# Kernel tuning notes

Measured on AMD Instinct MI355X. Metric: run time of the kernel, lower is better.

The kernel has to match this reference:

```python
import jax, jax.numpy as jnp
import numpy as np

N_HEAD = 16

def setup_inputs() -> dict:
    key = jax.random.key(0)
    k1, k2, k3, k4, k5 = jax.random.split(key, 5)
    B, T, C = 8, 2048, 1024
    hs = C // N_HEAD  # 64
    return {
        "ids": jax.random.normal(k1, (B, T, C), dtype=jnp.float32),
        "qkv_w": jax.random.normal(k2, (3 * hs, C), dtype=jnp.float32) * (C ** -0.5),
        "qkv_b": jax.random.normal(k3, (3 * hs,), dtype=jnp.float32) * 0.02,
        "proj_w": jax.random.normal(k4, (C, C), dtype=jnp.float32) * (C ** -0.5),
        "proj_b": jax.random.normal(k5, (C,), dtype=jnp.float32) * 0.02,
    }

def reference(ids, qkv_w, qkv_b, proj_w, proj_b):
    B, T, C = ids.shape
    hs = qkv_w.shape[0] // 3  # head_size
    # All heads share the same qkv Linear (input is replicated per-head in the
    # original), so compute one head and tile at the end.
    qkv = ids @ qkv_w.T + qkv_b                      # [B,T,3*hs]
    q, k, v = jnp.split(qkv, 3, axis=-1)             # each [B,T,hs]
    wei = jnp.einsum('btd,bsd->bts', q, k)           # [B,T,T]
    tril = jnp.tril(jnp.ones((T, T), dtype=bool))
    wei = jnp.where(tril, wei, jnp.float32(0.0))     # causal mask (no softmax)
    out_h = jnp.einsum('bts,bsd->btd', wei, v)       # [B,T,hs]
    out = jnp.tile(out_h, (1, 1, N_HEAD))            # identical heads concatenated
    return out @ proj_w.T + proj_b                   # [B,T,C]
```

## Files before the change

kernel.cpp:

```cpp
#include <hip/hip_runtime.h>
#include <hip/hip_bf16.h>

#define Bsz 8
#define Tsz 2048
#define Csz 1024
#define HSsz 64
#define NQ 192

typedef __attribute__((ext_vector_type(8))) short short8v;
typedef __attribute__((ext_vector_type(4))) float f32x4;
typedef unsigned short ushortT;
typedef unsigned int uintT;

__device__ __forceinline__ unsigned int f2bf(float f) {
    union { float f; unsigned int u; } v; v.f = f;
    return (v.u + 0x7fffu + ((v.u >> 16) & 1u)) >> 16;
}

__device__ __forceinline__ unsigned int pk2bf(float lo, float hi) {
    union { __hip_bfloat162 h2; unsigned int u; } cv;
    cv.h2 = __float22bfloat162_rn(float2{lo, hi});
    return cv.u;
}

__global__ __launch_bounds__(256) void k_prep(const float* __restrict__ qw,
                                              const float* __restrict__ pw,
                                              ushortT* __restrict__ wB,
                                              ushortT* __restrict__ w2a) {
    const int blk = blockIdx.x;
    if (blk < 96) {
        int idx = blk * 256 + threadIdx.x;
        int l = idx & 63;
        int ksjt = idx >> 6;
        int jt = ksjt % 12, ks = ksjt / 12;
        int j = jt * 16 + (l & 15);
        int k = ks * 32 + (l >> 4) * 8;
        const float* src = &qw[j * Csz + k];
        float4 a = *(const float4*)src;
        float4 b = *(const float4*)(src + 4);
        uint4 o;
        o.x = f2bf(a.x) | (f2bf(a.y) << 16);
        o.y = f2bf(a.z) | (f2bf(a.w) << 16);
        o.z = f2bf(b.x) | (f2bf(b.y) << 16);
        o.w = f2bf(b.z) | (f2bf(b.w) << 16);
        *(uint4*)&wB[(size_t)idx * 8] = o;
    } else {
        int idx = (blk - 96) * 256 + threadIdx.x;
        int l = idx & 63;
        int rest = idx >> 6;
        int m = rest & 63, ks = rest >> 6;
        int c = m * 16 + (l & 15);
        int d0 = ks * 32 + (l >> 4) * 8;
        float s0 = 0, s1 = 0, s2 = 0, s3 = 0, s4 = 0, s5 = 0, s6 = 0, s7 = 0;
#pragma unroll
        for (int hh = 0; hh < 16; ++hh) {
            const float* p = &pw[c * Csz + hh * HSsz + d0];
            float4 x = *(const float4*)p;
            float4 y = *(const float4*)(p + 4);
            s0 += x.x; s1 += x.y; s2 += x.z; s3 += x.w;
            s4 += y.x; s5 += y.y; s6 += y.z; s7 += y.w;
        }
        uint4 o;
        o.x = f2bf(s0) | (f2bf(s1) << 16);
        o.y = f2bf(s2) | (f2bf(s3) << 16);
        o.z = f2bf(s4) | (f2bf(s5) << 16);
        o.w = f2bf(s6) | (f2bf(s7) << 16);
        *(uint4*)&w2a[(size_t)idx * 8] = o;
    }
}

__global__ __launch_bounds__(512, 4) void k_qkv_mfma(const float* __restrict__ ids,
                                                     const ushortT* __restrict__ wB,
                                                     const float* __restrict__ bias,
                                                     ushortT* __restrict__ Qf,
                                                     ushortT* __restrict__ Kf,
                                                     ushortT* __restrict__ Vf) {
    __shared__ float sA[2][32 * 132];
    uintT* Lqk = (uintT*)&sA[0][0];
    uintT* Lv  = Lqk + 32 * 68;

    const int tid = threadIdx.x;
    const int wv  = tid >> 6;
    const int l   = tid & 63;
    const int wm  = wv >> 2;
    const int wn  = wv & 3;
    const int lg  = l >> 4, ll = l & 15;

    const int row0 = blockIdx.x * 32;

    const int srow = tid >> 4;
    const int scol = (tid & 15) * 8;
    const float* gsrc = ids + (size_t)(row0 + srow) * Csz + scol;

    const int afrow = wm * 16 + ll;

    f32x4 acc[3];
    acc[0] = acc[1] = acc[2] = (f32x4){0.f, 0.f, 0.f, 0.f};

    float4 st0 = *(const float4*)gsrc;
    float4 st1 = *(const float4*)(gsrc + 4);

    const ushortT* bbase_p = wB + ((size_t)(wn * 3) * 64 + l) * 8;

    for (int c = 0; c < 8; ++c) {
        float* bufp = &sA[c & 1][0];
        float* wp = &bufp[srow * 132 + scol];
        *(float4*)wp = st0;
        *(float4*)(wp + 4) = st1;
        __syncthreads();
        if (c < 7) {
            st0 = *(const float4*)(gsrc + (c + 1) * 128);
            st1 = *(const float4*)(gsrc + (c + 1) * 128 + 4);
        }
#pragma unroll
        for (int kk = 0; kk < 4; ++kk) {
            const ushortT* bp = bbase_p + (size_t)(4 * c + kk) * 6144;
            short8v b0 = *(const short8v*)(bp);
            short8v b1 = *(const short8v*)(bp + 512);
            short8v b2 = *(const short8v*)(bp + 1024);

            const float* ap = &bufp[afrow * 132 + kk * 32 + lg * 8];
            float4 a0 = *(const float4*)ap;
            float4 a1 = *(const float4*)(ap + 4);
            union { short8v s; unsigned int u[4]; } af;
            af.u[0] = pk2bf(a0.x, a0.y); af.u[1] = pk2bf(a0.z, a0.w);
            af.u[2] = pk2bf(a1.x, a1.y); af.u[3] = pk2bf(a1.z, a1.w);

            acc[0] = __builtin_amdgcn_mfma_f32_16x16x32_bf16(af.s, b0, acc[0], 0, 0, 0);
            acc[1] = __builtin_amdgcn_mfma_f32_16x16x32_bf16(af.s, b1, acc[1], 0, 0, 0);
            acc[2] = __builtin_amdgcn_mfma_f32_16x16x32_bf16(af.s, b2, acc[2], 0, 0, 0);
        }
    }
    __syncthreads();

    const int crow_l = wm * 16 + lg * 4;
    ushortT* L16 = (ushortT*)Lqk;
#pragma unroll
    for (int n = 0; n < 3; ++n) {
        const int jb = wn * 3 + n;
        const int j  = jb * 16 + ll;
        const float bj = bias[j];
        float v0 = acc[n][0] + bj, v1 = acc[n][1] + bj;
        float v2 = acc[n][2] + bj, v3 = acc[n][3] + bj;
        if (jb < 8) {
            ushortT* p = &L16[crow_l * 136 + j];
            p[0]   = (ushortT)f2bf(v0);
            p[136] = (ushortT)f2bf(v1);
            p[272] = (ushortT)f2bf(v2);
            p[408] = (ushortT)f2bf(v3);
        } else {
            uintT* p = &Lv[(j - 128) * 20 + (crow_l >> 1)];
            p[0] = pk2bf(v0, v1);
            p[1] = pk2bf(v2, v3);
        }
    }
    __syncthreads();

    const int l2 = tid & 63, ll2 = l2 & 15, lg2 = l2 >> 4;
    if (tid < 256) {
        const int ks = (tid >> 6) & 1, m = tid >> 7;
        uint4 q = *(const uint4*)&Lqk[(m * 16 + ll2) * 68 + ks * 16 + lg2 * 4];
        *(uint4*)&Qf[(((size_t)(row0 >> 4) + m) * 2 + ks) * 512 + l2 * 8] = q;
        const int n = tid >> 6;
        uint4 v = *(const uint4*)&Lv[(n * 16 + ll2) * 20 + lg2 * 4];
        const int bb = row0 >> 11, s32 = (row0 >> 5) & 63;
        *(uint4*)&Vf[((((size_t)bb * 64 + s32) * 4 + n) * 64 + l2) * 8] = v;
    } else {
        const int ks = (tid >> 6) & 1, m = (tid >> 7) & 1;
        uint4 k = *(const uint4*)&Lqk[(m * 16 + ll2) * 68 + 32 + ks * 16 + lg2 * 4];
        *(uint4*)&Kf[(((size_t)(row0 >> 4) + m) * 2 + ks) * 512 + l2 * 8] = k;
    }
}

__global__ __launch_bounds__(256, 3) void k_attn_mfma(const ushortT* __restrict__ Qf,
                                                      const ushortT* __restrict__ Kf,
                                                      const ushortT* __restrict__ Vf,
                                                      ushortT* __restrict__ hf) {
    __shared__ uintT su[4 * 2 * 16 * 36];
    __shared__ float s_o[4][32 * 68];

    const int tid = threadIdx.x;
    const int w  = tid >> 6;
    const int l  = tid & 63;
    const int lg = l >> 4;
    const int ll = l & 15;

    const int u = blockIdx.x;
    const int b = u & 7;
    const int si = 63 - (u >> 3);

    const int nT  = (si >> 1) + 1;
    const int qn  = nT >> 2, rem = nT & 3;
    const int t0  = w * qn + (w < rem ? w : rem);
    const int cnt = qn + (w < rem ? 1 : 0);

    const int gq = b * 128 + si * 2;

    short8v qf[2][2];
#pragma unroll
    for (int mt = 0; mt < 2; ++mt)
#pragma unroll
        for (int ks = 0; ks < 2; ++ks)
            qf[mt][ks] = *(const short8v*)&Qf[(((size_t)gq + mt) * 2 + ks) * 512 + l * 8];

    f32x4 oacc[2][4];
#pragma unroll
    for (int mt = 0; mt < 2; ++mt)
#pragma unroll
        for (int n = 0; n < 4; ++n) oacc[mt][n] = (f32x4){0.f, 0.f, 0.f, 0.f};

    for (int tile = t0; tile < t0 + cnt; ++tile) {
        const int gs = b * 128 + tile * 4;
        short8v kf[4][2];
#pragma unroll
        for (int ms = 0; ms < 4; ++ms) {
            const ushortT* kp = &Kf[(((size_t)gs + ms) * 2) * 512 + l * 8];
            kf[ms][0] = *(const short8v*)kp;
            kf[ms][1] = *(const short8v*)(kp + 512);
        }
        f32x4 sacc[4][2];
#pragma unroll
        for (int ms = 0; ms < 4; ++ms)
#pragma unroll
            for (int mt = 0; mt < 2; ++mt) sacc[ms][mt] = (f32x4){0.f, 0.f, 0.f, 0.f};
#pragma unroll
        for (int ms = 0; ms < 4; ++ms)
#pragma unroll
            for (int mt = 0; mt < 2; ++mt) {
                sacc[ms][mt] = __builtin_amdgcn_mfma_f32_16x16x32_bf16(kf[ms][0], qf[mt][0], sacc[ms][mt], 0, 0, 0);
                sacc[ms][mt] = __builtin_amdgcn_mfma_f32_16x16x32_bf16(kf[ms][1], qf[mt][1], sacc[ms][mt], 0, 0, 0);
            }
        if (tile == nT - 1) {
#pragma unroll
            for (int ms = 0; ms < 4; ++ms)
#pragma unroll
                for (int mt = 0; mt < 2; ++mt) {
                    const int tg = si * 32 + mt * 16 + ll;
#pragma unroll
                    for (int rr2 = 0; rr2 < 4; ++rr2) {
                        int sg = tile * 64 + ms * 16 + 4 * lg + rr2;
                        if (sg > tg) sacc[ms][mt][rr2] = 0.f;
                    }
                }
        }
#pragma unroll
        for (int mt = 0; mt < 2; ++mt)
#pragma unroll
            for (int ms = 0; ms < 4; ++ms) {
                uint2 pk;
                pk.x = pk2bf(sacc[ms][mt][0], sacc[ms][mt][1]);
                pk.y = pk2bf(sacc[ms][mt][2], sacc[ms][mt][3]);
                *(uint2*)&su[((w * 2 + mt) * 16 + ll) * 36 + ms * 8 + 2 * lg] = pk;
            }
        union { uint4 u4; short8v s; } pa[2][2];
#pragma unroll
        for (int mt = 0; mt < 2; ++mt)
#pragma unroll
            for (int h = 0; h < 2; ++h)
                pa[mt][h].u4 = *(const uint4*)&su[((w * 2 + mt) * 16 + ll) * 36 + h * 16 + lg * 4];

        const int gv = b * 64 + tile * 2;
        short8v vf[2][4];
#pragma unroll
        for (int h = 0; h < 2; ++h)
#pragma unroll
            for (int n = 0; n < 4; ++n)
                vf[h][n] = *(const short8v*)&Vf[((((size_t)gv + h) * 4 + n) * 64 + l) * 8];
#pragma unroll
        for (int mt = 0; mt < 2; ++mt)
#pragma unroll
            for (int n = 0; n < 4; ++n) {
                oacc[mt][n] = __builtin_amdgcn_mfma_f32_16x16x32_bf16(pa[mt][0].s, vf[0][n], oacc[mt][n], 0, 0, 0);
                oacc[mt][n] = __builtin_amdgcn_mfma_f32_16x16x32_bf16(pa[mt][1].s, vf[1][n], oacc[mt][n], 0, 0, 0);
            }
    }

#pragma unroll
    for (int mt = 0; mt < 2; ++mt)
#pragma unroll
        for (int n = 0; n < 4; ++n)
#pragma unroll
            for (int rr2 = 0; rr2 < 4; ++rr2)
                s_o[w][(mt * 16 + 4 * lg + rr2) * 68 + 16 * n + ll] = oacc[mt][n][rr2];
    __syncthreads();

    const int l2 = tid & 63, ll2 = l2 & 15, lg2 = l2 >> 4;
    const int ks = (tid >> 6) & 1, mt = tid >> 7;
    const int t = mt * 16 + ll2, dd = ks * 32 + lg2 * 8;
    float4 A = {0, 0, 0, 0}, B2 = {0, 0, 0, 0};
#pragma unroll
    for (int w2 = 0; w2 < 4; ++w2) {
        const float4 x = *(const float4*)&s_o[w2][t * 68 + dd];
        const float4 y = *(const float4*)&s_o[w2][t * 68 + dd + 4];
        A.x += x.x; A.y += x.y; A.z += x.z; A.w += x.w;
        B2.x += y.x; B2.y += y.y; B2.z += y.z; B2.w += y.w;
    }
    uint4 o;
    o.x = pk2bf(A.x, A.y);  o.y = pk2bf(A.z, A.w);
    o.z = pk2bf(B2.x, B2.y); o.w = pk2bf(B2.z, B2.w);
    *(uint4*)&hf[(((size_t)(b * 128 + si * 2) + mt) * 2 + ks) * 512 + l2 * 8] = o;
}

__global__ __launch_bounds__(256) void k_proj_mfma(const ushortT* __restrict__ hf,
                                                   const ushortT* __restrict__ w2a,
                                                   const float* __restrict__ pb,
                                                   float* __restrict__ out) {
    const int tid = threadIdx.x;
    const int w = tid >> 6, l = tid & 63;
    const size_t M0 = (size_t)blockIdx.x * 2;

    short8v hA0 = *(const short8v*)&hf[(M0 * 2 + 0) * 512 + l * 8];
    short8v hA1 = *(const short8v*)&hf[(M0 * 2 + 1) * 512 + l * 8];
    short8v hB0 = *(const short8v*)&hf[((M0 + 1) * 2 + 0) * 512 + l * 8];
    short8v hB1 = *(const short8v*)&hf[((M0 + 1) * 2 + 1) * 512 + l * 8];

    const int row = (l >> 4) * 4;
    const int tcol = l & 15;
    const size_t outA = (M0 * 16 + tcol) * Csz;
    const size_t outB = ((M0 + 1) * 16 + tcol) * Csz;

#pragma unroll 2
    for (int m = w * 16; m < w * 16 + 16; ++m) {
        const ushortT* ap = w2a + (size_t)(m * 64 + l) * 8;
        short8v a0 = *(const short8v*)ap;
        short8v a1 = *(const short8v*)(ap + 32768);
        const int c0 = m * 16 + row;
        const float4 pv = *(const float4*)&pb[c0];

        f32x4 accA = (f32x4){0.f, 0.f, 0.f, 0.f};
        accA = __builtin_amdgcn_mfma_f32_16x16x32_bf16(a0, hA0, accA, 0, 0, 0);
        accA = __builtin_amdgcn_mfma_f32_16x16x32_bf16(a1, hA1, accA, 0, 0, 0);
        f32x4 accB = (f32x4){0.f, 0.f, 0.f, 0.f};
        accB = __builtin_amdgcn_mfma_f32_16x16x32_bf16(a0, hB0, accB, 0, 0, 0);
        accB = __builtin_amdgcn_mfma_f32_16x16x32_bf16(a1, hB1, accB, 0, 0, 0);

        float4 oA, oB;
        oA.x = accA[0] + pv.x; oA.y = accA[1] + pv.y;
        oA.z = accA[2] + pv.z; oA.w = accA[3] + pv.w;
        oB.x = accB[0] + pv.x; oB.y = accB[1] + pv.y;
        oB.z = accB[2] + pv.z; oB.w = accB[3] + pv.w;
        *(float4*)&out[outA + c0] = oA;
        *(float4*)&out[outB + c0] = oB;
    }
}

extern "C" void kernel_launch(void* const* d_in, const int* in_sizes, int n_in,
                              void* d_out, int out_size, void* d_ws, size_t ws_size,
                              hipStream_t stream) {
    const float* ids    = (const float*)d_in[0];
    const float* qkv_w  = (const float*)d_in[1];
    const float* qkv_b  = (const float*)d_in[2];
    const float* proj_w = (const float*)d_in[3];
    const float* proj_b = (const float*)d_in[4];
    float* out = (float*)d_out;

    ushortT* Qf  = (ushortT*)d_ws;
    ushortT* Kf  = Qf + 16384 * HSsz;
    ushortT* Vf  = Kf + 16384 * HSsz;
    ushortT* hf  = Vf + 16384 * HSsz;
    ushortT* wB  = hf + 16384 * HSsz;
    ushortT* w2a = wB + 196608;

    hipLaunchKernelGGL(k_prep,      dim3(128), dim3(256), 0, stream, qkv_w, proj_w, wB, w2a);
    hipLaunchKernelGGL(k_qkv_mfma,  dim3(512), dim3(512), 0, stream, ids, wB, qkv_b, Qf, Kf, Vf);
    hipLaunchKernelGGL(k_attn_mfma, dim3(512), dim3(256), 0, stream, Qf, Kf, Vf, hf);
    hipLaunchKernelGGL(k_proj_mfma, dim3(512), dim3(256), 0, stream, hf, w2a, proj_b, out);
}
```

Measured before the change: 60.16 us.

## Double QKV row tile to 64 and stage activations as bf16 in LDS

```diff
diff --git a/kernel.cpp b/kernel.cpp
--- a/kernel.cpp
+++ b/kernel.cpp
@@ -75,60 +75,61 @@
                                                      ushortT* __restrict__ Qf,
                                                      ushortT* __restrict__ Kf,
                                                      ushortT* __restrict__ Vf) {
-    __shared__ float sA[2][32 * 132];
-    uintT* Lqk = (uintT*)&sA[0][0];
-    uintT* Lv  = Lqk + 32 * 68;
+    __shared__ uintT sA[2][64 * 68];
+    uintT* Lqk = &sA[0][0];
+    uintT* Lv  = Lqk + 64 * 68;
 
     const int tid = threadIdx.x;
     const int wv  = tid >> 6;
     const int l   = tid & 63;
-    const int wm  = wv >> 2;
-    const int wn  = wv & 3;
+    const int wm  = wv >> 1;
+    const int wn  = wv & 1;
     const int lg  = l >> 4, ll = l & 15;
 
-    const int row0 = blockIdx.x * 32;
-
-    const int srow = tid >> 4;
-    const int scol = (tid & 15) * 8;
+    const int row0 = blockIdx.x * 64;
+
+    const int srow = tid >> 3;
+    const int scol = (tid & 7) * 4;
     const float* gsrc = ids + (size_t)(row0 + srow) * Csz + scol;
+    const int swbase = srow * 68 + (scol >> 1);
 
     const int afrow = wm * 16 + ll;
 
-    f32x4 acc[3];
-    acc[0] = acc[1] = acc[2] = (f32x4){0.f, 0.f, 0.f, 0.f};
-
-    float4 st0 = *(const float4*)gsrc;
-    float4 st1 = *(const float4*)(gsrc + 4);
-
-    const ushortT* bbase_p = wB + ((size_t)(wn * 3) * 64 + l) * 8;
+    f32x4 acc[6];
+#pragma unroll
+    for (int n = 0; n < 6; ++n) acc[n] = (f32x4){0.f, 0.f, 0.f, 0.f};
+
+    float4 st[4];
+#pragma unroll
+    for (int j = 0; j < 4; ++j) st[j] = *(const float4*)(gsrc + j * 32);
+
+    const ushortT* bbase_p = wB + ((size_t)(wn * 6) * 64 + l) * 8;
 
     for (int c = 0; c < 8; ++c) {
-        float* bufp = &sA[c & 1][0];
-        float* wp = &bufp[srow * 132 + scol];
-        *(float4*)wp = st0;
-        *(float4*)(wp + 4) = st1;
+        uintT* bufp = &sA[c & 1][0];
+#pragma unroll
+        for (int j = 0; j < 4; ++j) {
+            uint2 pk;
+            pk.x = pk2bf(st[j].x, st[j].y);
+            pk.y = pk2bf(st[j].z, st[j].w);
+            *(uint2*)&bufp[swbase + j * 16] = pk;
+        }
         __syncthreads();
         if (c < 7) {
-            st0 = *(const float4*)(gsrc + (c + 1) * 128);
-            st1 = *(const float4*)(gsrc + (c + 1) * 128 + 4);
+#pragma unroll
+            for (int j = 0; j < 4; ++j)
+                st[j] = *(const float4*)(gsrc + (c + 1) * 128 + j * 32);
         }
 #pragma unroll
         for (int kk = 0; kk < 4; ++kk) {
             const ushortT* bp = bbase_p + (size_t)(4 * c + kk) * 6144;
-            short8v b0 = *(const short8v*)(bp);
-            short8v b1 = *(const short8v*)(bp + 512);
-            short8v b2 = *(const short8v*)(bp + 1024);
-
-            const float* ap = &bufp[afrow * 132 + kk * 32 + lg * 8];
-            float4 a0 = *(const float4*)ap;
-            float4 a1 = *(const float4*)(ap + 4);
-            union { short8v s; unsigned int u[4]; } af;
-            af.u[0] = pk2bf(a0.x, a0.y); af.u[1] = pk2bf(a0.z, a0.w);
-            af.u[2] = pk2bf(a1.x, a1.y); af.u[3] = pk2bf(a1.z, a1.w);
-
-            acc[0] = __builtin_amdgcn_mfma_f32_16x16x32_bf16(af.s, b0, acc[0], 0, 0, 0);
-            acc[1] = __builtin_amdgcn_mfma_f32_16x16x32_bf16(af.s, b1, acc[1], 0, 0, 0);
-            acc[2] = __builtin_amdgcn_mfma_f32_16x16x32_bf16(af.s, b2, acc[2], 0, 0, 0);
+            union { uint4 u4; short8v s; } af;
+            af.u4 = *(const uint4*)&bufp[afrow * 68 + kk * 16 + lg * 4];
+#pragma unroll
+            for (int n = 0; n < 6; ++n) {
+                short8v bf_ = *(const short8v*)(bp + n * 512);
+                acc[n] = __builtin_amdgcn_mfma_f32_16x16x32_bf16(af.s, bf_, acc[n], 0, 0, 0);
+            }
         }
     }
     __syncthreads();
@@ -136,8 +137,8 @@
     const int crow_l = wm * 16 + lg * 4;
     ushortT* L16 = (ushortT*)Lqk;
 #pragma unroll
-    for (int n = 0; n < 3; ++n) {
-        const int jb = wn * 3 + n;
+    for (int n = 0; n < 6; ++n) {
+        const int jb = wn * 6 + n;
         const int j  = jb * 16 + ll;
         const float bj = bias[j];
         float v0 = acc[n][0] + bj, v1 = acc[n][1] + bj;
@@ -149,7 +150,7 @@
             p[272] = (ushortT)f2bf(v2);
             p[408] = (ushortT)f2bf(v3);
         } else {
-            uintT* p = &Lv[(j - 128) * 20 + (crow_l >> 1)];
+            uintT* p = &Lv[(j - 128) * 36 + (crow_l >> 1)];
             p[0] = pk2bf(v0, v1);
             p[1] = pk2bf(v2, v3);
         }
@@ -157,18 +158,18 @@
     __syncthreads();
 
     const int l2 = tid & 63, ll2 = l2 & 15, lg2 = l2 >> 4;
-    if (tid < 256) {
+    {
         const int ks = (tid >> 6) & 1, m = tid >> 7;
         uint4 q = *(const uint4*)&Lqk[(m * 16 + ll2) * 68 + ks * 16 + lg2 * 4];
         *(uint4*)&Qf[(((size_t)(row0 >> 4) + m) * 2 + ks) * 512 + l2 * 8] = q;
-        const int n = tid >> 6;
-        uint4 v = *(const uint4*)&Lv[(n * 16 + ll2) * 20 + lg2 * 4];
-        const int bb = row0 >> 11, s32 = (row0 >> 5) & 63;
-        *(uint4*)&Vf[((((size_t)bb * 64 + s32) * 4 + n) * 64 + l2) * 8] = v;
-    } else {
-        const int ks = (tid >> 6) & 1, m = (tid >> 7) & 1;
         uint4 k = *(const uint4*)&Lqk[(m * 16 + ll2) * 68 + 32 + ks * 16 + lg2 * 4];
         *(uint4*)&Kf[(((size_t)(row0 >> 4) + m) * 2 + ks) * 512 + l2 * 8] = k;
+    }
+    {
+        const int g = tid >> 8, n = (tid >> 6) & 3;
+        uint4 v = *(const uint4*)&Lv[(n * 16 + ll2) * 36 + g * 16 + lg2 * 4];
+        const int bb = row0 >> 11, s32 = (row0 >> 5) & 63;
+        *(uint4*)&Vf[((((size_t)bb * 64 + s32 + g) * 4 + n) * 64 + l2) * 8] = v;
     }
 }
 
@@ -362,7 +363,7 @@
     ushortT* w2a = wB + 196608;
 
     hipLaunchKernelGGL(k_prep,      dim3(128), dim3(256), 0, stream, qkv_w, proj_w, wB, w2a);
-    hipLaunchKernelGGL(k_qkv_mfma,  dim3(512), dim3(512), 0, stream, ids, wB, qkv_b, Qf, Kf, Vf);
+    hipLaunchKernelGGL(k_qkv_mfma,  dim3(256), dim3(512), 0, stream, ids, wB, qkv_b, Qf, Kf, Vf);
     hipLaunchKernelGGL(k_attn_mfma, dim3(512), dim3(256), 0, stream, Qf, Kf, Vf, hf);
     hipLaunchKernelGGL(k_proj_mfma, dim3(512), dim3(256), 0, stream, hf, w2a, proj_b, out);
 }
```

Measured after the change: 78.51 us. 30.5% more time.
